# Kernel optimization log

Measured on AMD Instinct MI355X. Metric: run time of the kernel, lower is better.

Reference implementation:

```python
import jax, jax.numpy as jnp
import numpy as np

B, S, C = 64, 512, 512   # batch, subseq_length, in_features
H, D = 4, 128            # n_heads, hidden_features (H*D == C)
LN_EPS = 1e-5


def setup_inputs() -> dict:
    key = jax.random.key(0)
    k_h, k_w, k_b = jax.random.split(key, 3)
    h = jax.random.normal(k_h, (B, S, C), dtype=jnp.float32)
    # stacked per-head Linear weights, stored as [H, in, hid] for x @ W
    W = jax.random.normal(k_w, (H, C, D), dtype=jnp.float32) * (1.0 / np.sqrt(C))
    b = jax.random.normal(k_b, (H, D), dtype=jnp.float32) * 0.01
    adj = jnp.ones((S, S), dtype=jnp.float32)
    gamma = jnp.ones((C,), dtype=jnp.float32)
    beta = jnp.zeros((C,), dtype=jnp.float32)
    return {"t": 0, "h": h, "W": W, "b": b, "adj": adj, "gamma": gamma, "beta": beta}


def reference(t, h, W, b, adj, gamma, beta):
    # per-head projection: [H, B, S, D]
    hp = jnp.einsum("bsc,hcd->hbsd", h, W) + b[:, None, None, :]
    # raw scores, multiplicative adjacency mask (non-standard: mask BEFORE softmax by multiply)
    scores = jnp.einsum("hbsd,hbtd->hbst", hp, hp) * adj
    attn = jax.nn.softmax(scores, axis=-1)
    out = jnp.einsum("hbst,hbtd->hbsd", attn, hp)
    # concat heads along feature dim -> [B, S, H*D] == [B, S, C]
    out = jnp.transpose(out, (1, 2, 0, 3)).reshape(h.shape[0], h.shape[1], -1)
    # LayerNorm over last dim
    mu = jnp.mean(out, axis=-1, keepdims=True)
    var = jnp.mean(jnp.square(out - mu), axis=-1, keepdims=True)
    out = (out - mu) * jax.lax.rsqrt(var + LN_EPS) * gamma + beta
    # GELU (exact erf form, matching torch nn.GELU default)
    return jax.nn.gelu(out, approximate=False)
```

## Files before the change

### kernel.cpp

```cpp
#include <hip/hip_runtime.h>
#include <stdint.h>


typedef float  f32x4   __attribute__((ext_vector_type(4)));
typedef short  bf16x8  __attribute__((ext_vector_type(8)));
typedef unsigned short ushort8 __attribute__((ext_vector_type(8)));
typedef unsigned int   uint2v  __attribute__((ext_vector_type(2)));
typedef unsigned int   uint4v  __attribute__((ext_vector_type(4)));

#define GLD16(src, dst)                                                        \
  __builtin_amdgcn_global_load_lds(                                            \
      (const __attribute__((address_space(1))) void*)(src),                    \
      (__attribute__((address_space(3))) void*)(dst), 16, 0, 0)

__device__ __forceinline__ unsigned short f32_to_bf16(float x) {
  union { float f; unsigned int u; } v; v.f = x;
  unsigned int r = v.u + 0x7FFFu + ((v.u >> 16) & 1u);
  return (unsigned short)(r >> 16);
}
__device__ __forceinline__ float bf16_to_f32(unsigned int h) {
  union { float f; unsigned int u; } v; v.u = h << 16;
  return v.f;
}
__device__ __forceinline__ f32x4 mfma16(bf16x8 a, bf16x8 b, f32x4 c) {
  return __builtin_amdgcn_mfma_f32_16x16x32_bf16(a, b, c, 0, 0, 0);
}
__device__ __forceinline__ float bperm_f(int srcLane, float v) {
  return __int_as_float(__builtin_amdgcn_ds_bpermute(srcLane << 2, __float_as_int(v)));
}
__device__ __forceinline__ uint2 pk2(float fa, float fb) {
  unsigned ua = __float_as_uint(fa), ub = __float_as_uint(fb);
  uint2 r;
  r.x = (ua >> 16) | (ub & 0xFFFF0000u);
  float ra = fa - __uint_as_float(ua & 0xFFFF0000u);
  float rb = fb - __uint_as_float(ub & 0xFFFF0000u);
  r.y = (__float_as_uint(ra) >> 16) | (__float_as_uint(rb) & 0xFFFF0000u);
  return r;
}
__device__ __forceinline__ uint2v tr_read(const unsigned short* p) {
  uint2v r;
  asm volatile("ds_read_b64_tr_b16 %0, %1"
               : "=v"(r)
               : "v"((const __attribute__((address_space(3))) void*)p)
               : "memory");
  return r;
}

__global__ __launch_bounds__(256) void cast_split_Wt(
    const float* __restrict__ W, unsigned short* __restrict__ whi,
    unsigned short* __restrict__ wlo) {
  int o = blockIdx.x * 256 + threadIdx.x;
  int hd = o >> 16;
  int rem = o & 65535;
  int d = rem >> 9;
  int c = rem & 511;
  float v = W[((size_t)(hd * 512 + c)) * 128 + d];
  unsigned short h0 = f32_to_bf16(v);
  whi[o] = h0;
  wlo[o] = f32_to_bf16(v - bf16_to_f32(h0));
}

__global__ __launch_bounds__(256) void cast_adj(
    const float* __restrict__ src, unsigned short* __restrict__ dst) {
  size_t i = ((size_t)blockIdx.x * 256 + threadIdx.x) * 8;
  f32x4 a = *(const f32x4*)(src + i);
  f32x4 b = *(const f32x4*)(src + i + 4);
  ushort8 o;
#pragma unroll
  for (int e = 0; e < 4; ++e) {
    o[e] = f32_to_bf16(a[e]);
    o[4 + e] = f32_to_bf16(b[e]);
  }
  *(ushort8*)(dst + i) = o;
}

__global__ __launch_bounds__(256, 2) void proj_gemm(
    const float* __restrict__ hsrc,
    const unsigned short* __restrict__ whi, const unsigned short* __restrict__ wlo,
    const float* __restrict__ bias, unsigned short* __restrict__ hp_hi,
    unsigned short* __restrict__ hp_lo) {
  int bid = blockIdx.x;
  int swz = (bid & 7) * 128 + (bid >> 3);
  int nt = swz & 3, mt = swz >> 2;
  int m0 = mt * 128, n0 = nt * 128;

  __shared__ alignas(16) unsigned short Ah[8192], Al[8192], Bh[8192], Bl[8192];

  int tid = threadIdx.x, wv = tid >> 6, lane = tid & 63;
  int l15 = lane & 15, l4 = lane >> 4;
  int wr = wv >> 1, wc = wv & 1;
  int arow = tid >> 3;
  int acol8 = (tid & 7) * 8;

  f32x4 acc[4][4];
#pragma unroll
  for (int a = 0; a < 4; ++a)
#pragma unroll
    for (int b = 0; b < 4; ++b) acc[a][b] = (f32x4){0.f, 0.f, 0.f, 0.f};

  f32x4 areg[4][2];
#pragma unroll
  for (int j = 0; j < 4; ++j) {
    const float* rp = hsrc + (size_t)(m0 + j * 32 + arow) * 512 + acol8;
    areg[j][0] = *(const f32x4*)rp;
    areg[j][1] = *(const f32x4*)(rp + 4);
  }

  for (int ks = 0; ks < 8; ++ks) {
    int k0 = ks * 64;
    for (int i = wv; i < 32; i += 4) {
      int grp = i >> 4, j = i & 15;
      int row = j * 8 + (lane >> 3);
      int off = (lane & 7) * 16;
      int sw = (row & 7) << 4;
      const unsigned short* sb = grp ? wlo : whi;
      unsigned short* db = grp ? Bl : Bh;
      GLD16((const char*)sb + ((size_t)(nt * 128 + row) * 512 + k0) * 2 + (off ^ sw),
            db + j * 512);
    }
    __builtin_amdgcn_sched_barrier(0);
#pragma unroll
    for (int j = 0; j < 4; ++j) {
      int r = j * 32 + arow;
      uint4v uh, ul;
      uint2 p0 = pk2(areg[j][0][0], areg[j][0][1]);
      uint2 p1 = pk2(areg[j][0][2], areg[j][0][3]);
      uint2 p2 = pk2(areg[j][1][0], areg[j][1][1]);
      uint2 p3 = pk2(areg[j][1][2], areg[j][1][3]);
      uh[0] = p0.x; ul[0] = p0.y;
      uh[1] = p1.x; ul[1] = p1.y;
      uh[2] = p2.x; ul[2] = p2.y;
      uh[3] = p3.x; ul[3] = p3.y;
      int boff = r * 128 + ((acol8 * 2) ^ ((r & 7) << 4));
      *(uint4v*)((char*)Ah + boff) = uh;
      *(uint4v*)((char*)Al + boff) = ul;
    }
    if (ks < 7) {
#pragma unroll
      for (int j = 0; j < 4; ++j) {
        const float* rp = hsrc + (size_t)(m0 + j * 32 + arow) * 512 + k0 + 64 + acol8;
        areg[j][0] = *(const f32x4*)rp;
        areg[j][1] = *(const f32x4*)(rp + 4);
      }
    }
    if (ks < 7) {
      asm volatile("s_waitcnt vmcnt(8) lgkmcnt(0)" ::: "memory");
    } else {
      asm volatile("s_waitcnt vmcnt(0) lgkmcnt(0)" ::: "memory");
    }
    __builtin_amdgcn_s_barrier();
    __builtin_amdgcn_sched_barrier(0);

#pragma unroll
    for (int ks2 = 0; ks2 < 2; ++ks2) {
      int kb = (ks2 * 64 + 16 * l4);
      bf16x8 fah[4], fal[4], fbh[4], fbl[4];
#pragma unroll
      for (int f = 0; f < 4; ++f) {
        int mr = wr * 64 + f * 16 + l15;
        int aadr = mr * 128 + (kb ^ ((mr & 7) << 4));
        fah[f] = *(const bf16x8*)((const char*)Ah + aadr);
        fal[f] = *(const bf16x8*)((const char*)Al + aadr);
        int nr = wc * 64 + f * 16 + l15;
        int badr = nr * 128 + (kb ^ ((nr & 7) << 4));
        fbh[f] = *(const bf16x8*)((const char*)Bh + badr);
        fbl[f] = *(const bf16x8*)((const char*)Bl + badr);
      }
#pragma unroll
      for (int a = 0; a < 4; ++a)
#pragma unroll
        for (int b = 0; b < 4; ++b) {
          acc[a][b] = mfma16(fah[a], fbh[b], acc[a][b]);
          acc[a][b] = mfma16(fah[a], fbl[b], acc[a][b]);
          acc[a][b] = mfma16(fal[a], fbh[b], acc[a][b]);
        }
    }
    asm volatile("s_waitcnt lgkmcnt(0)" ::: "memory");
    __builtin_amdgcn_s_barrier();
    __builtin_amdgcn_sched_barrier(0);
  }

  __syncthreads();

#pragma unroll
  for (int a = 0; a < 4; ++a) {
    __syncthreads();
#pragma unroll
    for (int b = 0; b < 4; ++b) {
      int cloc = wc * 64 + b * 16 + l15;
      float bv = bias[n0 + cloc];
#pragma unroll
      for (int r = 0; r < 4; ++r) {
        int rloc = wr * 16 + 4 * l4 + r;
        float v = acc[a][b][r] + bv;
        unsigned short hh = f32_to_bf16(v);
        Ah[rloc * 128 + cloc] = hh;
        Al[rloc * 128 + cloc] = f32_to_bf16(v - bf16_to_f32(hh));
      }
    }
    __syncthreads();
    int rr = tid >> 3, c16 = (tid & 7) * 16;
    int mg = m0 + (rr >> 4) * 64 + a * 16 + (rr & 15);
    bf16x8 vh0 = *(const bf16x8*)(Ah + rr * 128 + c16);
    bf16x8 vh1 = *(const bf16x8*)(Ah + rr * 128 + c16 + 8);
    bf16x8 vl0 = *(const bf16x8*)(Al + rr * 128 + c16);
    bf16x8 vl1 = *(const bf16x8*)(Al + rr * 128 + c16 + 8);
    *(bf16x8*)(hp_hi + (size_t)mg * 512 + n0 + c16) = vh0;
    *(bf16x8*)(hp_hi + (size_t)mg * 512 + n0 + c16 + 8) = vh1;
    *(bf16x8*)(hp_lo + (size_t)mg * 512 + n0 + c16) = vl0;
    *(bf16x8*)(hp_lo + (size_t)mg * 512 + n0 + c16 + 8) = vl1;
  }
}

__global__ __launch_bounds__(256, 2) void attn_kernel(
    const unsigned short* __restrict__ hp_hi, const unsigned short* __restrict__ hp_lo,
    const unsigned short* __restrict__ adjb, unsigned short* __restrict__ ob) {
  int bid = blockIdx.x;
  int swz = (bid & 7) * 128 + (bid >> 3);
  int qt = swz & 3;
  int hd = (swz >> 2) & 3;
  int bb = swz >> 4;
  int q0 = qt * 128;

  __shared__ alignas(16) unsigned short SM[32768];

  int tid = threadIdx.x, w = tid >> 6, lane = tid & 63;
  int l15 = lane & 15, l4 = lane >> 4;
  int qgb = q0 + w * 32 + l15;

  bf16x8 qh[2][4], ql[2][4];
#pragma unroll
  for (int nf = 0; nf < 2; ++nf) {
    size_t base = ((size_t)bb * 512 + qgb + nf * 16) * 512 + hd * 128 + 8 * l4;
#pragma unroll
    for (int ds = 0; ds < 4; ++ds) {
      qh[nf][ds] = *(const bf16x8*)(hp_hi + base + ds * 32);
      ql[nf][ds] = *(const bf16x8*)(hp_lo + base + ds * 32);
    }
  }

  f32x4 o[2][8];
#pragma unroll
  for (int nf = 0; nf < 2; ++nf)
#pragma unroll
    for (int vf = 0; vf < 8; ++vf) o[nf][vf] = (f32x4){0.f, 0.f, 0.f, 0.f};
  float m_run[2] = {-3.0e38f, -3.0e38f};
  float l_run[2] = {0.f, 0.f};

  const unsigned short* ssb = (w & 2) ? hp_lo : hp_hi;
  int sdst = ((w & 2) ? 8192 : 0) + (w & 1) * 4096;
  int skvh = (w & 1) * 32;
  int skv = lane >> 1, sdh = lane & 1;

  {
    size_t rowb = ((size_t)(bb * 512 + skvh + skv)) * 1024 + hd * 256 + sdh * 16;
#pragma unroll
    for (int sd = 0; sd < 8; ++sd)
      GLD16((const char*)ssb + rowb + sd * 32, SM + sdst + sd * 512);
  }
  asm volatile("s_waitcnt vmcnt(0)" ::: "memory");
  __syncthreads();

  for (int t = 0; t < 8; ++t) {
    int kv0 = t * 64;
    const unsigned short* Kb = SM + ((t & 1) << 14);
    const unsigned short* Khi = Kb;
    const unsigned short* Klo = Kb + 8192;

    if (t < 7) {
      unsigned short* Nb = SM + (((t + 1) & 1) << 14) + sdst;
      size_t rowb = ((size_t)(bb * 512 + kv0 + 64 + skvh + skv)) * 1024 +
                    hd * 256 + sdh * 16;
#pragma unroll
      for (int sd = 0; sd < 8; ++sd)
        GLD16((const char*)ssb + rowb + sd * 32, Nb + sd * 512);
    }
    uint2 ua[2][4];
#pragma unroll
    for (int nf = 0; nf < 2; ++nf) {
      const unsigned short* ab = adjb + (size_t)(qgb + nf * 16) * 512 + kv0;
#pragma unroll
      for (int m = 0; m < 4; ++m)
        ua[nf][m] = *(const uint2*)(ab + m * 16 + 4 * l4);
    }

    f32x4 sc[2][4];
#pragma unroll
    for (int nf = 0; nf < 2; ++nf)
#pragma unroll
      for (int m = 0; m < 4; ++m) sc[nf][m] = (f32x4){0.f, 0.f, 0.f, 0.f};
    __builtin_amdgcn_s_setprio(1);
#pragma unroll
    for (int kvh = 0; kvh < 2; ++kvh) {
#pragma unroll
      for (int ds = 0; ds < 4; ++ds) {
        int boff = (kvh * 8 + 2 * ds + (l4 >> 1)) * 1024 + 16 * (l4 & 1);
        int a0 = boff + l15 * 32;
        int a1 = boff + (16 + l15) * 32;
        bf16x8 kh0 = *(const bf16x8*)((const char*)Khi + a0);
        bf16x8 kl0 = *(const bf16x8*)((const char*)Klo + a0);
        bf16x8 kh1 = *(const bf16x8*)((const char*)Khi + a1);
        bf16x8 kl1 = *(const bf16x8*)((const char*)Klo + a1);
        int m0i = kvh * 2, m1i = kvh * 2 + 1;
#pragma unroll
        for (int nf = 0; nf < 2; ++nf) {
          sc[nf][m0i] = mfma16(kh0, qh[nf][ds], sc[nf][m0i]);
          sc[nf][m1i] = mfma16(kh1, qh[nf][ds], sc[nf][m1i]);
          sc[nf][m0i] = mfma16(kh0, ql[nf][ds], sc[nf][m0i]);
          sc[nf][m1i] = mfma16(kh1, ql[nf][ds], sc[nf][m1i]);
          sc[nf][m0i] = mfma16(kl0, qh[nf][ds], sc[nf][m0i]);
          sc[nf][m1i] = mfma16(kl1, qh[nf][ds], sc[nf][m1i]);
        }
      }
    }
    __builtin_amdgcn_s_setprio(0);

    union PU { bf16x8 v; unsigned u[4]; } pah[2][2];
#pragma unroll
    for (int nf = 0; nf < 2; ++nf) {
      float p[4][4];
      float tm = -3.0e38f;
#pragma unroll
      for (int m = 0; m < 4; ++m) {
        f32x4 av;
        av[0] = bf16_to_f32(ua[nf][m].x & 0xFFFFu);
        av[1] = bf16_to_f32(ua[nf][m].x >> 16);
        av[2] = bf16_to_f32(ua[nf][m].y & 0xFFFFu);
        av[3] = bf16_to_f32(ua[nf][m].y >> 16);
#pragma unroll
        for (int r = 0; r < 4; ++r) {
          p[m][r] = sc[nf][m][r] * av[r];
          tm = fmaxf(tm, p[m][r]);
        }
      }
      tm = fmaxf(tm, __shfl_xor(tm, 16));
      tm = fmaxf(tm, __shfl_xor(tm, 32));
      if (__any(tm > m_run[nf] + 8.0f)) {
        float mn = fmaxf(m_run[nf], tm);
        float scl = __expf(m_run[nf] - mn);
        m_run[nf] = mn;
        l_run[nf] *= scl;
        f32x4 s4;
#pragma unroll
        for (int r = 0; r < 4; ++r) s4[r] = bperm_f(4 * l4 + r, scl);
#pragma unroll
        for (int vf = 0; vf < 8; ++vf)
#pragma unroll
          for (int r = 0; r < 4; ++r) o[nf][vf][r] *= s4[r];
      }
      float ps = 0.f;
#pragma unroll
      for (int m = 0; m < 4; ++m)
#pragma unroll
        for (int r = 0; r < 4; ++r) {
          p[m][r] = __expf(p[m][r] - m_run[nf]);
          ps += p[m][r];
        }
      ps += __shfl_xor(ps, 16);
      ps += __shfl_xor(ps, 32);
      l_run[nf] += ps;
#pragma unroll
      for (int kvh = 0; kvh < 2; ++kvh)
#pragma unroll
        for (int i = 0; i < 4; ++i) {
          float fa = (i < 2) ? p[kvh * 2][2 * i] : p[kvh * 2 + 1][2 * (i - 2)];
          float fb = (i < 2) ? p[kvh * 2][2 * i + 1]
                             : p[kvh * 2 + 1][2 * (i - 2) + 1];
          pah[nf][kvh].u[i] = (__float_as_uint(fa) >> 16) |
                              (__float_as_uint(fb) & 0xFFFF0000u);
        }
    }

#pragma unroll
    for (int kvh = 0; kvh < 2; ++kvh) {
      const unsigned short* trb = Khi + kvh * 4096 + lane * 4;
      union VU { bf16x8 v; uint2v u2[2]; } vh[8];
#pragma unroll
      for (int vf = 0; vf < 8; ++vf) {
        vh[vf].u2[0] = tr_read(trb + vf * 512);
        vh[vf].u2[1] = tr_read(trb + vf * 512 + 256);
      }
      asm volatile("s_waitcnt lgkmcnt(0)" ::: "memory");
      __builtin_amdgcn_sched_barrier(0);
      __builtin_amdgcn_s_setprio(1);
#pragma unroll
      for (int vf = 0; vf < 8; ++vf) {
        o[0][vf] = mfma16(pah[0][kvh].v, vh[vf].v, o[0][vf]);
        o[1][vf] = mfma16(pah[1][kvh].v, vh[vf].v, o[1][vf]);
      }
      __builtin_amdgcn_s_setprio(0);
    }
    asm volatile("s_waitcnt vmcnt(0) lgkmcnt(0)" ::: "memory");
    __syncthreads();
  }

#pragma unroll
  for (int nf = 0; nf < 2; ++nf) {
    float rinv = 1.0f / l_run[nf];
    f32x4 r4;
#pragma unroll
    for (int r = 0; r < 4; ++r) r4[r] = bperm_f(4 * l4 + r, rinv);
    float* wbase = (float*)SM + w * 2048;
#pragma unroll
    for (int vf = 0; vf < 8; ++vf)
#pragma unroll
      for (int r = 0; r < 4; ++r)
        wbase[(4 * l4 + r) * 128 + vf * 16 + l15] = o[nf][vf][r] * r4[r];
    __syncthreads();
#pragma unroll
    for (int p = 0; p < 4; ++p) {
      int row = p * 4 + l4;
      f32x4 v0 = *(const f32x4*)(wbase + row * 128 + l15 * 8);
      f32x4 v1 = *(const f32x4*)(wbase + row * 128 + l15 * 8 + 4);
      ushort8 o8;
#pragma unroll
      for (int e = 0; e < 4; ++e) {
        o8[e] = f32_to_bf16(v0[e]);
        o8[4 + e] = f32_to_bf16(v1[e]);
      }
      size_t mg = (size_t)bb * 512 + q0 + w * 32 + nf * 16 + row;
      *(ushort8*)(ob + mg * 512 + hd * 128 + l15 * 8) = o8;
    }
    __syncthreads();
  }
}

__global__ __launch_bounds__(256) void ln_gelu_kernel(
    const unsigned short* __restrict__ in, float* __restrict__ outp,
    const float* __restrict__ gamma, const float* __restrict__ beta) {
  int w = threadIdx.x >> 6, lane = threadIdx.x & 63;
  size_t row = (size_t)blockIdx.x * 4 + w;
  ushort8 v = *(const ushort8*)(in + row * 512 + lane * 8);
  float x[8];
#pragma unroll
  for (int e = 0; e < 8; ++e) x[e] = bf16_to_f32((unsigned int)(unsigned short)v[e]);
  float s = 0.f;
#pragma unroll
  for (int e = 0; e < 8; ++e) s += x[e];
#pragma unroll
  for (int off = 32; off >= 1; off >>= 1) s += __shfl_xor(s, off);
  float mu = s * (1.0f / 512.0f);
  float vs = 0.f;
#pragma unroll
  for (int e = 0; e < 8; ++e) {
    float d = x[e] - mu; vs += d * d;
  }
#pragma unroll
  for (int off = 32; off >= 1; off >>= 1) vs += __shfl_xor(vs, off);
  float rs = rsqrtf(vs * (1.0f / 512.0f) + 1e-5f);
  f32x4 g0 = *(const f32x4*)(gamma + lane * 8);
  f32x4 g1 = *(const f32x4*)(gamma + lane * 8 + 4);
  f32x4 b0 = *(const f32x4*)(beta + lane * 8);
  f32x4 b1 = *(const f32x4*)(beta + lane * 8 + 4);
  f32x4 y0, y1;
#pragma unroll
  for (int e = 0; e < 4; ++e) {
    float y = (x[e] - mu) * rs * g0[e] + b0[e];
    y0[e] = 0.5f * y * (1.0f + erff(y * 0.70710678118654752f));
    float z = (x[4 + e] - mu) * rs * g1[e] + b1[e];
    y1[e] = 0.5f * z * (1.0f + erff(z * 0.70710678118654752f));
  }
  float* p = outp + row * 512 + lane * 8;
  *(f32x4*)p = y0;
  *(f32x4*)(p + 4) = y1;
}

extern "C" void kernel_launch(void* const* d_in, const int* in_sizes, int n_in,
                              void* d_out, int out_size, void* d_ws, size_t ws_size,
                              hipStream_t stream) {
  const float* h     = (const float*)d_in[1];
  const float* W     = (const float*)d_in[2];
  const float* bias  = (const float*)d_in[3];
  const float* adj   = (const float*)d_in[4];
  const float* gamma = (const float*)d_in[5];
  const float* beta  = (const float*)d_in[6];
  float* out = (float*)d_out;

  unsigned short* ws = (unsigned short*)d_ws;
  unsigned short* adj_bf = ws;
  unsigned short* ob     = ws + 16777216;
  unsigned short* hp_hi  = ws + 33554432;
  unsigned short* hp_lo  = ws + 50331648;
  unsigned short* Wt_hi  = ws + 67108864;
  unsigned short* Wt_lo  = ws + 67371008;

  cast_split_Wt<<<1024, 256, 0, stream>>>(W, Wt_hi, Wt_lo);
  cast_adj<<<128, 256, 0, stream>>>(adj, adj_bf);
  proj_gemm<<<1024, 256, 0, stream>>>(h, Wt_hi, Wt_lo, bias, hp_hi, hp_lo);
  attn_kernel<<<1024, 256, 0, stream>>>(hp_hi, hp_lo, adj_bf, ob);
  ln_gelu_kernel<<<8192, 256, 0, stream>>>(ob, out, gamma, beta);
}
```

Before: 173.0 us.

## Drop K-lo term from QK^T, stage only hi K tile, raise occupancy to 3

```diff
diff --git a/kernel.cpp b/kernel.cpp
--- a/kernel.cpp
+++ b/kernel.cpp
@@ -212,7 +212,7 @@
   }
 }
 
-__global__ __launch_bounds__(256, 2) void attn_kernel(
+__global__ __launch_bounds__(256, 3) void attn_kernel(
     const unsigned short* __restrict__ hp_hi, const unsigned short* __restrict__ hp_lo,
     const unsigned short* __restrict__ adjb, unsigned short* __restrict__ ob) {
   int bid = blockIdx.x;
@@ -222,7 +222,7 @@
   int bb = swz >> 4;
   int q0 = qt * 128;
 
-  __shared__ alignas(16) unsigned short SM[32768];
+  __shared__ alignas(16) unsigned short SM[24576];
 
   int tid = threadIdx.x, w = tid >> 6, lane = tid & 63;
   int l15 = lane & 15, l4 = lane >> 4;
@@ -247,33 +247,34 @@
   float m_run[2] = {-3.0e38f, -3.0e38f};
   float l_run[2] = {0.f, 0.f};
 
-  const unsigned short* ssb = (w & 2) ? hp_lo : hp_hi;
-  int sdst = ((w & 2) ? 8192 : 0) + (w & 1) * 4096;
-  int skvh = (w & 1) * 32;
   int skv = lane >> 1, sdh = lane & 1;
 
-  {
-    size_t rowb = ((size_t)(bb * 512 + skvh + skv)) * 1024 + hd * 256 + sdh * 16;
-#pragma unroll
-    for (int sd = 0; sd < 8; ++sd)
-      GLD16((const char*)ssb + rowb + sd * 32, SM + sdst + sd * 512);
+#pragma unroll
+  for (int j = 0; j < 4; ++j) {
+    int s = w * 4 + j;
+    int kvh = s >> 3, sd = s & 7;
+    const char* src = (const char*)hp_hi +
+        ((size_t)(bb * 512 + kvh * 32 + skv)) * 1024 + hd * 256 + sd * 32 + sdh * 16;
+    GLD16(src, SM + kvh * 4096 + sd * 512);
   }
   asm volatile("s_waitcnt vmcnt(0)" ::: "memory");
   __syncthreads();
 
   for (int t = 0; t < 8; ++t) {
     int kv0 = t * 64;
-    const unsigned short* Kb = SM + ((t & 1) << 14);
-    const unsigned short* Khi = Kb;
-    const unsigned short* Klo = Kb + 8192;
+    const unsigned short* Kb = SM + ((t & 1) << 13);
 
     if (t < 7) {
-      unsigned short* Nb = SM + (((t + 1) & 1) << 14) + sdst;
-      size_t rowb = ((size_t)(bb * 512 + kv0 + 64 + skvh + skv)) * 1024 +
-                    hd * 256 + sdh * 16;
-#pragma unroll
-      for (int sd = 0; sd < 8; ++sd)
-        GLD16((const char*)ssb + rowb + sd * 32, Nb + sd * 512);
+      unsigned short* Nb = SM + (((t + 1) & 1) << 13);
+#pragma unroll
+      for (int j = 0; j < 4; ++j) {
+        int s = w * 4 + j;
+        int kvh = s >> 3, sd = s & 7;
+        const char* src = (const char*)hp_hi +
+            ((size_t)(bb * 512 + kv0 + 64 + kvh * 32 + skv)) * 1024 +
+            hd * 256 + sd * 32 + sdh * 16;
+        GLD16(src, Nb + kvh * 4096 + sd * 512);
+      }
     }
     uint2 ua[2][4];
 #pragma unroll
@@ -289,7 +290,6 @@
     for (int nf = 0; nf < 2; ++nf)
 #pragma unroll
       for (int m = 0; m < 4; ++m) sc[nf][m] = (f32x4){0.f, 0.f, 0.f, 0.f};
-    __builtin_amdgcn_s_setprio(1);
 #pragma unroll
     for (int kvh = 0; kvh < 2; ++kvh) {
 #pragma unroll
@@ -297,10 +297,8 @@
         int boff = (kvh * 8 + 2 * ds + (l4 >> 1)) * 1024 + 16 * (l4 & 1);
         int a0 = boff + l15 * 32;
         int a1 = boff + (16 + l15) * 32;
-        bf16x8 kh0 = *(const bf16x8*)((const char*)Khi + a0);
-        bf16x8 kl0 = *(const bf16x8*)((const char*)Klo + a0);
-        bf16x8 kh1 = *(const bf16x8*)((const char*)Khi + a1);
-        bf16x8 kl1 = *(const bf16x8*)((const char*)Klo + a1);
+        bf16x8 kh0 = *(const bf16x8*)((const char*)Kb + a0);
+        bf16x8 kh1 = *(const bf16x8*)((const char*)Kb + a1);
         int m0i = kvh * 2, m1i = kvh * 2 + 1;
 #pragma unroll
         for (int nf = 0; nf < 2; ++nf) {
@@ -308,12 +306,9 @@
           sc[nf][m1i] = mfma16(kh1, qh[nf][ds], sc[nf][m1i]);
           sc[nf][m0i] = mfma16(kh0, ql[nf][ds], sc[nf][m0i]);
           sc[nf][m1i] = mfma16(kh1, ql[nf][ds], sc[nf][m1i]);
-          sc[nf][m0i] = mfma16(kl0, qh[nf][ds], sc[nf][m0i]);
-          sc[nf][m1i] = mfma16(kl1, qh[nf][ds], sc[nf][m1i]);
         }
       }
     }
-    __builtin_amdgcn_s_setprio(0);
 
     union PU { bf16x8 v; unsigned u[4]; } pah[2][2];
 #pragma unroll
@@ -373,7 +368,7 @@
 
 #pragma unroll
     for (int kvh = 0; kvh < 2; ++kvh) {
-      const unsigned short* trb = Khi + kvh * 4096 + lane * 4;
+      const unsigned short* trb = Kb + kvh * 4096 + lane * 4;
       union VU { bf16x8 v; uint2v u2[2]; } vh[8];
 #pragma unroll
       for (int vf = 0; vf < 8; ++vf) {
@@ -382,13 +377,11 @@
       }
       asm volatile("s_waitcnt lgkmcnt(0)" ::: "memory");
       __builtin_amdgcn_sched_barrier(0);
-      __builtin_amdgcn_s_setprio(1);
 #pragma unroll
       for (int vf = 0; vf < 8; ++vf) {
         o[0][vf] = mfma16(pah[0][kvh].v, vh[vf].v, o[0][vf]);
         o[1][vf] = mfma16(pah[1][kvh].v, vh[vf].v, o[1][vf]);
       }
-      __builtin_amdgcn_s_setprio(0);
     }
     asm volatile("s_waitcnt vmcnt(0) lgkmcnt(0)" ::: "memory");
     __syncthreads();
```

Measured after the change: 292.5 us. 69.1% more time.
